# Kernel optimization log

Measured on AMD Instinct MI355X. Metric: run time of the kernel, lower is better.

Reference implementation:

```python
import jax, jax.numpy as jnp
import numpy as np

B, N, C, H = 4, 2048, 1024, 16
D = C // H  # head dim


def setup_inputs() -> dict:
    key = jax.random.key(0)
    ks = jax.random.split(key, 9)
    s = 1.0 / np.sqrt(C)
    inp = {"x": jax.random.normal(ks[0], (B, N, C), dtype=jnp.float32)}
    names = ["wq", "wk", "wv", "wo"]
    for i, n in enumerate(names):
        inp[n] = jax.random.uniform(ks[1 + 2 * i], (C, C), dtype=jnp.float32, minval=-s, maxval=s)
        inp["b" + n[1]] = jax.random.uniform(ks[2 + 2 * i], (C,), dtype=jnp.float32, minval=-s, maxval=s)
    return inp


def reference(x, wq, bq, wk, bk, wv, bv, wo, bo):
    b, n, c = x.shape
    # projections; weights stored as (in, out) so y = x @ w + b
    def split_heads(y):
        return y.reshape(b, n, H, D).transpose(0, 2, 1, 3)  # (B,H,N,D)

    q = split_heads(x @ wq + bq)
    k = split_heads(x @ wk + bk)
    v = split_heads(x @ wv + bv)
    scores = jnp.einsum("bhnd,bhmd->bhnm", q, k) / np.sqrt(D).astype(x.dtype)
    attn = jax.nn.softmax(scores, axis=-1)
    ctx = jnp.einsum("bhnm,bhmd->bhnd", attn, v)
    out = ctx.transpose(0, 2, 1, 3).reshape(b, n, c)
    return out @ wo + bo
```

## Files before the change

kernel.cpp:

```cpp
#include <hip/hip_runtime.h>
#include <hip/hip_bf16.h>
#include <hip/hip_fp16.h>

#define SEQ 2048
#define NH  16
#define DH  64
#define CH  1024
#define BATCH 4
#define BH (BATCH*NH)
#define MTOK (BATCH*SEQ)

typedef unsigned short u16;
typedef _Float16 h8 __attribute__((ext_vector_type(8)));
typedef float f4 __attribute__((ext_vector_type(4)));
typedef float f16x __attribute__((ext_vector_type(16)));

#define AS1(p) ((const __attribute__((address_space(1))) unsigned int*)(p))
#define AS3(p) ((__attribute__((address_space(3))) unsigned int*)(p))

__device__ __forceinline__ u16 f2h(float f) {
  _Float16 h = (_Float16)f;
  return __builtin_bit_cast(unsigned short, h);
}

__device__ __forceinline__ unsigned cvtpk(float a, float b) {
  auto t = __builtin_amdgcn_cvt_pkrtz(a, b);
  return __builtin_bit_cast(unsigned, t);
}

__device__ __forceinline__ float ex2(float x) { return __builtin_amdgcn_exp2f(x); }

__device__ __forceinline__ float max16_3(const f16x& v) {
  float a = fmaxf(fmaxf(v[0], v[1]), v[2]);
  float b = fmaxf(fmaxf(v[3], v[4]), v[5]);
  float c = fmaxf(fmaxf(v[6], v[7]), v[8]);
  float d = fmaxf(fmaxf(v[9], v[10]), v[11]);
  float e = fmaxf(fmaxf(v[12], v[13]), v[14]);
  float f = fmaxf(fmaxf(a, b), v[15]);
  return fmaxf(fmaxf(fmaxf(c, d), e), f);
}

__global__ __launch_bounds__(256) void k_convert_x(const float* __restrict__ x,
                                                   u16* __restrict__ xh) {
  int idx = (blockIdx.x * 256 + threadIdx.x) * 8;
  float4 a = *(const float4*)(x + idx);
  float4 b = *(const float4*)(x + idx + 4);
  uint4 o;
  o.x = (unsigned)f2h(a.x) | ((unsigned)f2h(a.y) << 16);
  o.y = (unsigned)f2h(a.z) | ((unsigned)f2h(a.w) << 16);
  o.z = (unsigned)f2h(b.x) | ((unsigned)f2h(b.y) << 16);
  o.w = (unsigned)f2h(b.z) | ((unsigned)f2h(b.w) << 16);
  *(uint4*)(xh + idx) = o;
}

__global__ __launch_bounds__(256) void k_transpose_w(const float* __restrict__ w0,
                                                     const float* __restrict__ w1,
                                                     const float* __restrict__ w2,
                                                     const float* __restrict__ w3,
                                                     u16* __restrict__ dst_all) {
  int mat = blockIdx.z;
  const float* src = (mat == 0) ? w0 : (mat == 1) ? w1 : (mat == 2) ? w2 : w3;
  u16* dst = dst_all + (size_t)mat * (CH * CH);
  __shared__ float t[64][65];
  int n0 = blockIdx.x * 64, k0 = blockIdx.y * 64;
#pragma unroll
  for (int i = 0; i < 16; ++i) {
    int idx = threadIdx.x + i * 256;
    int r = idx >> 6, c = idx & 63;
    t[r][c] = src[(size_t)(k0 + r) * CH + n0 + c];
  }
  __syncthreads();
#pragma unroll
  for (int i = 0; i < 16; ++i) {
    int idx = threadIdx.x + i * 256;
    int r = idx >> 6, c = idx & 63;
    dst[(size_t)(n0 + r) * CH + k0 + c] = f2h(t[c][r]);
  }
}

__global__ __launch_bounds__(256) void k_transpose_v(const u16* __restrict__ v,
                                                     u16* __restrict__ vt) {
  int n0 = blockIdx.x * 64;
  int bh = blockIdx.y;
  __shared__ u16 t[64][68];
  const u16* src = v + (size_t)bh * SEQ * DH + (size_t)n0 * DH;
#pragma unroll
  for (int i = 0; i < 4; ++i) {
    int g = threadIdx.x + i * 256;
    int r = g >> 4, c4 = (g & 15) * 4;
    *(ushort4*)&t[r][c4] = *(const ushort4*)(src + (size_t)r * DH + c4);
  }
  __syncthreads();
  u16* dst = vt + (size_t)bh * DH * SEQ + n0;
#pragma unroll
  for (int i = 0; i < 4; ++i) {
    int g = threadIdx.x + i * 256;
    int d = g >> 4, k4 = (g & 15) * 4;
    ushort4 o;
    o.x = t[k4 + 0][d]; o.y = t[k4 + 1][d]; o.z = t[k4 + 2][d]; o.w = t[k4 + 3][d];
    *(ushort4*)(dst + (size_t)d * SEQ + k4) = o;
  }
}

__global__ __launch_bounds__(256) void k_gemm_qkv(
    const u16* __restrict__ xh, const u16* __restrict__ wt,
    const float* __restrict__ bq, const float* __restrict__ bk,
    const float* __restrict__ bv,
    u16* __restrict__ qo, u16* __restrict__ ko, u16* __restrict__ vo) {
  const int tid = threadIdx.x;
  const int lane = tid & 63;
  const int wv = tid >> 6;
  const int wr = wv >> 1, wc = wv & 1;
  const int l16 = lane & 15, g = lane >> 4;
  const int tm = blockIdx.x;
  const int tn = blockIdx.y;
  const int mat = tn >> 3;
  const int nbase = (tn & 7) * 128;
  const u16* wb = wt + (size_t)mat * (CH * CH);

  __shared__ u16 As[128 * 32];
  __shared__ u16 Bs[128 * 32];

  f4 zero = {0.f, 0.f, 0.f, 0.f};
  f4 acc[4][4];
#pragma unroll
  for (int m = 0; m < 4; ++m)
#pragma unroll
    for (int n = 0; n < 4; ++n) acc[m][n] = zero;

  for (int k0 = 0; k0 < CH; k0 += 32) {
#pragma unroll
    for (int j = 0; j < 2; ++j) {
      int rbase = wv * 32 + j * 16;
      int row = rbase + (lane >> 2);
      int blk = (lane & 3) ^ ((row >> 1) & 3);
      const u16* ga = xh + (size_t)(tm * 128 + row) * CH + k0 + blk * 8;
      __builtin_amdgcn_global_load_lds(AS1(ga), AS3(&As[rbase * 32]), 16, 0, 0);
      const u16* gb = wb + (size_t)(nbase + row) * CH + k0 + blk * 8;
      __builtin_amdgcn_global_load_lds(AS1(gb), AS3(&Bs[rbase * 32]), 16, 0, 0);
    }
    __syncthreads();

    h8 af[4], bf[4];
#pragma unroll
    for (int i = 0; i < 4; ++i) {
      int arow = wr * 64 + i * 16 + l16;
      af[i] = *(const h8*)&As[arow * 32 + ((g ^ ((arow >> 1) & 3)) * 8)];
      int brow = wc * 64 + i * 16 + l16;
      bf[i] = *(const h8*)&Bs[brow * 32 + ((g ^ ((brow >> 1) & 3)) * 8)];
    }
#pragma unroll
    for (int m = 0; m < 4; ++m)
#pragma unroll
      for (int n = 0; n < 4; ++n)
        acc[m][n] = __builtin_amdgcn_mfma_f32_16x16x32_f16(af[m], bf[n], acc[m][n], 0, 0, 0);
    __syncthreads();
  }

  const float* bias = (mat == 0) ? bq : (mat == 1) ? bk : bv;
  u16* outp = (mat == 0) ? qo : (mat == 1) ? ko : vo;
  const float qscale = (mat == 0) ? 0.125f * 1.44269504f : 1.0f;
#pragma unroll
  for (int n = 0; n < 4; ++n) {
    int col = nbase + wc * 64 + n * 16 + l16;
    float bcol = bias[col];
    int h_ = col >> 6, d_ = col & 63;
#pragma unroll
    for (int m = 0; m < 4; ++m) {
#pragma unroll
      for (int r = 0; r < 4; ++r) {
        int t = tm * 128 + wr * 64 + m * 16 + g * 4 + r;
        int b_ = t >> 11, nseq = t & 2047;
        float val = (acc[m][n][r] + bcol) * qscale;
        outp[(((size_t)(b_ * NH + h_) * SEQ) + nseq) * DH + d_] = f2h(val);
      }
    }
  }
}

__global__ __launch_bounds__(256, 4) void k_attn(const u16* __restrict__ q,
                                                 const u16* __restrict__ k,
                                                 const u16* __restrict__ vt,
                                                 u16* __restrict__ ctx) {
  const int qb0 = blockIdx.x;
  const int bh = blockIdx.y;
  const int tid = threadIdx.x;
  const int lane = tid & 63;
  const int w = tid >> 6;
  const int l31 = lane & 31;
  const int hi = lane >> 5;

  __shared__ u16 Ks[2][32 * 128];
  __shared__ u16 Vs[2][32 * 128];

  const u16* kbase = k + (size_t)bh * SEQ * DH;
  const u16* vbase = vt + (size_t)bh * DH * SEQ;
  const u16* qbase = q + (size_t)bh * SEQ * DH;
  const int q0 = qb0 * 128 + w * 32;

  h8 qf[4];
#pragma unroll
  for (int ds = 0; ds < 4; ++ds)
    qf[ds] = *(const h8*)(qbase + (size_t)(q0 + l31) * DH + 16 * ds + 8 * hi);

  int koff[2][4];
  int voff[2][2][2];
#pragma unroll
  for (int h = 0; h < 2; ++h) {
#pragma unroll
    for (int ds = 0; ds < 4; ++ds) {
      int slot = 8 * h + 2 * ds + hi;
      koff[h][ds] = l31 * 128 + ((slot ^ (l31 & 15)) * 8);
    }
#pragma unroll
    for (int db = 0; db < 2; ++db)
#pragma unroll
      for (int ks = 0; ks < 2; ++ks) {
        int slot = 8 * db + 4 * h + 2 * ks + hi;
        voff[h][db][ks] = l31 * 128 + ((slot ^ (l31 & 15)) * 8);
      }
  }

  const u16* gk[2];
  const u16* gv[2];
#pragma unroll
  for (int c = 0; c < 2; ++c) {
    int r2 = w * 8 + c * 4 + (lane >> 4);
    int S = (lane & 15) ^ (r2 & 15);
    gk[c] = kbase + (size_t)(r2 + 32 * (S >> 3)) * DH + (S & 7) * 8;
    gv[c] = vbase + (size_t)(r2 + 32 * (S >> 3)) * SEQ + (S & 7) * 8;
  }

  f16x accq[2];
  accq[0] = {}; accq[1] = {};
  float m0 = 0.f, l0 = 0.f;

  auto STAGE = [&](int bi) {
#pragma unroll
    for (int c = 0; c < 2; ++c) {
      __builtin_amdgcn_global_load_lds(AS1(gk[c]), AS3(&Ks[bi][(w * 8 + c * 4) * 128]), 16, 0, 0);
      __builtin_amdgcn_global_load_lds(AS1(gv[c]), AS3(&Vs[bi][(w * 8 + c * 4) * 128]), 16, 0, 0);
      gk[c] += 64 * DH;
      gv[c] += 64;
    }
  };

  auto pack8 = [&](const float* p, int ks) -> h8 {
    unsigned a0 = cvtpk(p[8 * ks + 0], p[8 * ks + 1]);
    unsigned c0 = cvtpk(p[8 * ks + 2], p[8 * ks + 3]);
    unsigned b0 = cvtpk(p[8 * ks + 4], p[8 * ks + 5]);
    unsigned d0 = cvtpk(p[8 * ks + 6], p[8 * ks + 7]);
    unsigned s1 = __shfl_xor(hi ? a0 : b0, 32, 64);
    unsigned s2 = __shfl_xor(hi ? c0 : d0, 32, 64);
    uint4 wds;
    wds.x = hi ? s1 : a0;
    wds.y = hi ? s2 : c0;
    wds.z = hi ? b0 : s1;
    wds.w = hi ? d0 : s2;
    return __builtin_bit_cast(h8, wds);
  };

  auto SUBSTEP = [&](const u16* Kb, const u16* Vb, int h) {
    f16x s = {};
#pragma unroll
    for (int ds = 0; ds < 4; ++ds) {
      h8 kf = *(const h8*)(Kb + koff[h][ds]);
      s = __builtin_amdgcn_mfma_f32_32x32x16_f16(kf, qf[ds], s, 0, 0, 0);
    }
    float tmx = max16_3(s);
    if (!__all(tmx <= m0 + 8.f)) {
      float tm2 = fmaxf(tmx, __shfl_xor(tmx, 32, 64));
      float mn = fmaxf(m0, tm2);
      float sc = ex2(m0 - mn);
      m0 = mn; l0 *= sc;
#pragma unroll
      for (int r = 0; r < 16; ++r) {
        int src = (lane & 32) + ((r & 3) + 8 * (r >> 2) + 4 * hi);
        float scr = __shfl(sc, src, 64);
        accq[0][r] *= scr; accq[1][r] *= scr;
      }
    }
    float p[16];
    float rs = 0.f;
#pragma unroll
    for (int r = 0; r < 16; ++r) { p[r] = ex2(s[r] - m0); rs += p[r]; }
    l0 += rs;

    h8 pa0 = pack8(p, 0);
    h8 pa1 = pack8(p, 1);
#pragma unroll
    for (int db = 0; db < 2; ++db) {
      h8 vf0 = *(const h8*)(Vb + voff[h][db][0]);
      accq[db] = __builtin_amdgcn_mfma_f32_32x32x16_f16(pa0, vf0, accq[db], 0, 0, 0);
      h8 vf1 = *(const h8*)(Vb + voff[h][db][1]);
      accq[db] = __builtin_amdgcn_mfma_f32_32x32x16_f16(pa1, vf1, accq[db], 0, 0, 0);
    }
  };

  STAGE(0);
  for (int kt = 0; kt < SEQ / 64; kt += 2) {
    __syncthreads();
    STAGE(1);
    SUBSTEP(&Ks[0][0], &Vs[0][0], 0);
    SUBSTEP(&Ks[0][0], &Vs[0][0], 1);
    __syncthreads();
    if (kt + 2 < SEQ / 64) STAGE(0);
    SUBSTEP(&Ks[1][0], &Vs[1][0], 0);
    SUBSTEP(&Ks[1][0], &Vs[1][0], 1);
  }

  l0 += __shfl_xor(l0, 32, 64);
  float inv0 = 1.0f / l0;
  int b_ = bh >> 4, h_ = bh & 15;
#pragma unroll
  for (int r = 0; r < 16; ++r) {
    int row = (r & 3) + 8 * (r >> 2) + 4 * hi;
    int src = (lane & 32) + row;
    float i0 = __shfl(inv0, src, 64);
#pragma unroll
    for (int db = 0; db < 2; ++db) {
      ctx[((size_t)(b_ * SEQ + q0 + row)) * CH + h_ * 64 + 32 * db + l31] =
          f2h(accq[db][r] * i0);
    }
  }
}

__global__ __launch_bounds__(256) void k_gemm_out(const u16* __restrict__ ctxb,
                                                  const u16* __restrict__ wot,
                                                  const float* __restrict__ bo,
                                                  float* __restrict__ out) {
  const int tid = threadIdx.x;
  const int lane = tid & 63;
  const int wv = tid >> 6;
  const int wr = wv >> 1, wc = wv & 1;
  const int l16 = lane & 15, g = lane >> 4;
  const int tm = blockIdx.x;
  const int nbase = blockIdx.y * 128;

  __shared__ u16 As[128 * 32];
  __shared__ u16 Bs[128 * 32];

  f4 zero = {0.f, 0.f, 0.f, 0.f};
  f4 acc[4][4];
#pragma unroll
  for (int m = 0; m < 4; ++m)
#pragma unroll
    for (int n = 0; n < 4; ++n) acc[m][n] = zero;

  for (int k0 = 0; k0 < CH; k0 += 32) {
#pragma unroll
    for (int j = 0; j < 2; ++j) {
      int rbase = wv * 32 + j * 16;
      int row = rbase + (lane >> 2);
      int blk = (lane & 3) ^ ((row >> 1) & 3);
      const u16* ga = ctxb + (size_t)(tm * 128 + row) * CH + k0 + blk * 8;
      __builtin_amdgcn_global_load_lds(AS1(ga), AS3(&As[rbase * 32]), 16, 0, 0);
      const u16* gb = wot + (size_t)(nbase + row) * CH + k0 + blk * 8;
      __builtin_amdgcn_global_load_lds(AS1(gb), AS3(&Bs[rbase * 32]), 16, 0, 0);
    }
    __syncthreads();

    h8 af[4], bf[4];
#pragma unroll
    for (int i = 0; i < 4; ++i) {
      int arow = wr * 64 + i * 16 + l16;
      af[i] = *(const h8*)&As[arow * 32 + ((g ^ ((arow >> 1) & 3)) * 8)];
      int brow = wc * 64 + i * 16 + l16;
      bf[i] = *(const h8*)&Bs[brow * 32 + ((g ^ ((brow >> 1) & 3)) * 8)];
    }
#pragma unroll
    for (int m = 0; m < 4; ++m)
#pragma unroll
      for (int n = 0; n < 4; ++n)
        acc[m][n] = __builtin_amdgcn_mfma_f32_16x16x32_f16(af[m], bf[n], acc[m][n], 0, 0, 0);
    __syncthreads();
  }

#pragma unroll
  for (int n = 0; n < 4; ++n) {
    int col = nbase + wc * 64 + n * 16 + l16;
    float bcol = bo[col];
#pragma unroll
    for (int m = 0; m < 4; ++m) {
#pragma unroll
      for (int r = 0; r < 4; ++r) {
        int t = tm * 128 + wr * 64 + m * 16 + g * 4 + r;
        out[(size_t)t * CH + col] = acc[m][n][r] + bcol;
      }
    }
  }
}

extern "C" void kernel_launch(void* const* d_in, const int* in_sizes, int n_in,
                              void* d_out, int out_size, void* d_ws, size_t ws_size,
                              hipStream_t stream) {
  (void)in_sizes; (void)n_in; (void)out_size; (void)ws_size;
  const float* x  = (const float*)d_in[0];
  const float* wq = (const float*)d_in[1];
  const float* bq = (const float*)d_in[2];
  const float* wk = (const float*)d_in[3];
  const float* bk = (const float*)d_in[4];
  const float* wv = (const float*)d_in[5];
  const float* bv = (const float*)d_in[6];
  const float* wo = (const float*)d_in[7];
  const float* bo = (const float*)d_in[8];
  float* out = (float*)d_out;

  char* ws = (char*)d_ws;
  u16* xh   = (u16*)(ws);
  u16* wt   = (u16*)(ws + 16777216);
  u16* qbuf = (u16*)(ws + 25165824);
  u16* kbuf = (u16*)(ws + 41943040);
  u16* vbuf = (u16*)(ws + 58720256);
  u16* ctxb = (u16*)(ws + 75497472);
  u16* wot  = wt + 3 * CH * CH;
  u16* vtb  = xh;

  k_convert_x<<<dim3(4096), dim3(256), 0, stream>>>(x, xh);
  k_transpose_w<<<dim3(16, 16, 4), dim3(256), 0, stream>>>(wq, wk, wv, wo, wt);
  k_gemm_qkv<<<dim3(64, 24), dim3(256), 0, stream>>>(xh, wt, bq, bk, bv, qbuf, kbuf, vbuf);
  k_transpose_v<<<dim3(32, 64), dim3(256), 0, stream>>>(vbuf, vtb);
  k_attn<<<dim3(16, 64), dim3(256), 0, stream>>>(qbuf, kbuf, vtb, ctxb);
  k_gemm_out<<<dim3(64, 8), dim3(256), 0, stream>>>(ctxb, wot, bo, out);
}
```

Measured before the change: 237.8 us.

## Compute softmax row sums via MFMA, remap attention grid, add MFMA priority hints

Computes the softmax denominator with extra MFMAs against a ones vector, replacing the scalar per-lane accumulation and the final cross-lane shuffles. Adds s_setprio around MFMA sections, skips the max subtraction while the running max is still zero, and flattens the attention grid with a swizzled block-to-(bh, query-block) mapping meant to improve L2 locality across XCDs. The aim is to cut VALU work in the softmax inner loop, at the cost of two extra MFMAs per substep and added register pressure for lsum.

```diff
diff --git a/kernel.cpp b/kernel.cpp
--- a/kernel.cpp
+++ b/kernel.cpp
@@ -182,8 +182,9 @@
                                                  const u16* __restrict__ k,
                                                  const u16* __restrict__ vt,
                                                  u16* __restrict__ ctx) {
-  const int qb0 = blockIdx.x;
-  const int bh = blockIdx.y;
+  const int bid = blockIdx.x;
+  const int bh = ((bid & 7) << 3) | ((bid >> 3) & 7);
+  const int qb0 = bid >> 6;
   const int tid = threadIdx.x;
   const int lane = tid & 63;
   const int w = tid >> 6;
@@ -231,9 +232,19 @@
     gv[c] = vbase + (size_t)(r2 + 32 * (S >> 3)) * SEQ + (S & 7) * 8;
   }
 
+  const f16x fzero = {};
+  h8 vones;
+  {
+    unsigned o1 = 0x3C003C00u;
+    uint4 t = {o1, o1, o1, o1};
+    vones = __builtin_bit_cast(h8, t);
+  }
+
   f16x accq[2];
   accq[0] = {}; accq[1] = {};
-  float m0 = 0.f, l0 = 0.f;
+  f16x lsum = {};
+  float m0 = 0.f;
+  bool virgin = true;
 
   auto STAGE = [&](int bi) {
 #pragma unroll
@@ -261,33 +272,42 @@
   };
 
   auto SUBSTEP = [&](const u16* Kb, const u16* Vb, int h) {
-    f16x s = {};
-#pragma unroll
-    for (int ds = 0; ds < 4; ++ds) {
+    h8 kf0 = *(const h8*)(Kb + koff[h][0]);
+    __builtin_amdgcn_s_setprio(1);
+    f16x s = __builtin_amdgcn_mfma_f32_32x32x16_f16(kf0, qf[0], fzero, 0, 0, 0);
+#pragma unroll
+    for (int ds = 1; ds < 4; ++ds) {
       h8 kf = *(const h8*)(Kb + koff[h][ds]);
       s = __builtin_amdgcn_mfma_f32_32x32x16_f16(kf, qf[ds], s, 0, 0, 0);
     }
+    __builtin_amdgcn_s_setprio(0);
     float tmx = max16_3(s);
+    tmx = fmaxf(tmx, __shfl_xor(tmx, 32, 64));
     if (!__all(tmx <= m0 + 8.f)) {
-      float tm2 = fmaxf(tmx, __shfl_xor(tmx, 32, 64));
-      float mn = fmaxf(m0, tm2);
+      float mn = fmaxf(m0, tmx);
       float sc = ex2(m0 - mn);
-      m0 = mn; l0 *= sc;
+      m0 = mn; virgin = false;
 #pragma unroll
       for (int r = 0; r < 16; ++r) {
         int src = (lane & 32) + ((r & 3) + 8 * (r >> 2) + 4 * hi);
         float scr = __shfl(sc, src, 64);
-        accq[0][r] *= scr; accq[1][r] *= scr;
+        accq[0][r] *= scr; accq[1][r] *= scr; lsum[r] *= scr;
       }
     }
     float p[16];
-    float rs = 0.f;
-#pragma unroll
-    for (int r = 0; r < 16; ++r) { p[r] = ex2(s[r] - m0); rs += p[r]; }
-    l0 += rs;
+    if (virgin) {
+#pragma unroll
+      for (int r = 0; r < 16; ++r) p[r] = ex2(s[r]);
+    } else {
+#pragma unroll
+      for (int r = 0; r < 16; ++r) p[r] = ex2(s[r] - m0);
+    }
 
     h8 pa0 = pack8(p, 0);
     h8 pa1 = pack8(p, 1);
+    __builtin_amdgcn_s_setprio(1);
+    lsum = __builtin_amdgcn_mfma_f32_32x32x16_f16(pa0, vones, lsum, 0, 0, 0);
+    lsum = __builtin_amdgcn_mfma_f32_32x32x16_f16(pa1, vones, lsum, 0, 0, 0);
 #pragma unroll
     for (int db = 0; db < 2; ++db) {
       h8 vf0 = *(const h8*)(Vb + voff[h][db][0]);
@@ -295,6 +315,7 @@
       h8 vf1 = *(const h8*)(Vb + voff[h][db][1]);
       accq[db] = __builtin_amdgcn_mfma_f32_32x32x16_f16(pa1, vf1, accq[db], 0, 0, 0);
     }
+    __builtin_amdgcn_s_setprio(0);
   };
 
   STAGE(0);
@@ -309,14 +330,11 @@
     SUBSTEP(&Ks[1][0], &Vs[1][0], 1);
   }
 
-  l0 += __shfl_xor(l0, 32, 64);
-  float inv0 = 1.0f / l0;
   int b_ = bh >> 4, h_ = bh & 15;
 #pragma unroll
   for (int r = 0; r < 16; ++r) {
     int row = (r & 3) + 8 * (r >> 2) + 4 * hi;
-    int src = (lane & 32) + row;
-    float i0 = __shfl(inv0, src, 64);
+    float i0 = 1.0f / lsum[r];
 #pragma unroll
     for (int db = 0; db < 2; ++db) {
       ctx[((size_t)(b_ * SEQ + q0 + row)) * CH + h_ * 64 + 32 * db + l31] =
@@ -420,6 +438,6 @@
   k_transpose_w<<<dim3(16, 16, 4), dim3(256), 0, stream>>>(wq, wk, wv, wo, wt);
   k_gemm_qkv<<<dim3(64, 24), dim3(256), 0, stream>>>(xh, wt, bq, bk, bv, qbuf, kbuf, vbuf);
   k_transpose_v<<<dim3(32, 64), dim3(256), 0, stream>>>(vbuf, vtb);
-  k_attn<<<dim3(16, 64), dim3(256), 0, stream>>>(qbuf, kbuf, vtb, ctxb);
+  k_attn<<<dim3(1024), dim3(256), 0, stream>>>(qbuf, kbuf, vtb, ctxb);
   k_gemm_out<<<dim3(64, 8), dim3(256), 0, stream>>>(ctxb, wot, bo, out);
 }
```

Measured after the change: 206.2 us. 13.3% less time.
